# Kernel optimization log

Hardware: AMD Instinct MI355X
Metric: run time of the kernel (lower is better)

## Reference

```python
import jax, jax.numpy as jnp
from jax import lax
import numpy as np

B, H, W = 8, 512, 512
HW = H * W  # sentinel label for non-mask pixels


def _label_components(mask):
    """4-connectivity connected-component labeling (min flat-index per component).
    mask: [H,W] bool. Returns [HW] int32 labels; non-mask pixels get label HW.
    Label propagation + pointer jumping -> O(log diameter) iterations."""
    idx = jnp.arange(HW, dtype=jnp.int32).reshape(H, W)
    lab0 = jnp.where(mask, idx, HW)

    def step(lab):
        p = jnp.pad(lab, 1, mode='constant', constant_values=HW)
        nb = jnp.minimum(jnp.minimum(p[:-2, 1:-1], p[2:, 1:-1]),
                         jnp.minimum(p[1:-1, :-2], p[1:-1, 2:]))
        new = jnp.where(mask, jnp.minimum(lab, nb), HW)
        flat = new.reshape(-1)
        flat_ext = jnp.concatenate([flat, jnp.array([HW], dtype=flat.dtype)])
        new = jnp.minimum(flat, flat_ext[flat]).reshape(H, W)  # pointer jump
        return jnp.where(mask, new, HW)

    def cond(state):
        return state[1]

    def body(state):
        lab, _ = state
        new = step(lab)
        return new, jnp.any(new != lab)

    lab, _ = lax.while_loop(cond, body, (lab0, jnp.array(True)))
    return lab.reshape(-1)


def _keep_large(mask):
    """Keep pixels belonging to components with area > max_area/2 (matches
    ndi.label + ndi.sum + thresholded relabel; ndi.sum scaling by 255/1 cancels)."""
    labels = _label_components(mask)  # [HW]
    counts = jax.ops.segment_sum(mask.reshape(-1).astype(jnp.float32), labels,
                                 num_segments=HW + 1)  # counts[HW]=0 (non-mask contributes 0)
    max_area = counts.max()
    keep = mask.reshape(-1) & (counts[labels] > 0.5 * max_area)
    return keep.reshape(mask.shape)


def _masked_ce(logits, target):
    """CrossEntropyLoss(ignore_index=255, reduction='mean'). logits [B,C,H,W], target [B,H,W]."""
    logp = jax.nn.log_softmax(logits, axis=1)
    valid = target != 255
    tc = jnp.where(valid, target, 0)
    nll = -jnp.take_along_axis(logp, tc[:, None], axis=1)[:, 0]  # [B,H,W]
    denom = jnp.maximum(jnp.sum(valid), 1).astype(logp.dtype)
    return jnp.sum(jnp.where(valid, nll, 0.0)) / denom


def setup_inputs() -> dict:
    key = jax.random.key(0)
    k1, k2 = jax.random.split(key)
    preds = jax.random.normal(k1, (3, B, 2, H, W), dtype=jnp.float32)
    cams = jax.random.uniform(k2, (B, 1, H, W), dtype=jnp.float32)
    return {"preds": preds, "cams": cams}


def reference(preds, cams):
    cam = cams[:, 0]                      # [B,H,W]
    bg_mask = cam >= 0.2                  # pixels left at 255 in bg_label (the labeled regions)
    fg_mask = cam > 0.6                   # pixels set to 1 in fg_label
    keep_bg = jax.vmap(_keep_large)(bg_mask)
    keep_fg = jax.vmap(_keep_large)(fg_mask)
    bg_t = jnp.where(keep_bg, 255, 0).astype(jnp.int32)   # large uncertain regions ignored
    fg_t = jnp.where(keep_fg, 1, 255).astype(jnp.int32)   # small/non-fg ignored
    loss = jnp.float32(0.0)
    for i in range(preds.shape[0]):       # weight (1**i / 1) == 1
        loss = loss + _masked_ce(preds[i], fg_t) + _masked_ce(preds[i], bg_t)
    return loss
```

## Files before the change

### kernel.cpp

```cpp
#include <hip/hip_runtime.h>
#include <hip/hip_bf16.h>
#include <math.h>

#define Bsz    8
#define Wdim   512
#define HWv    (512 * 512)
#define LOG2HW 18
#define NIMG   16
#define TILE   64
#define TPIX   (TILE * TILE)


__device__ __forceinline__ int uf_find(int* L, int x) {
  int p = L[x];
  while (p != x) {
    int gp = L[p];
    if (gp != p) atomicMin(&L[x], gp);
    x = gp;
    p = L[x];
  }
  return x;
}

__device__ __forceinline__ int find_ro(const int* __restrict__ L, int x) {
  int p = L[x];
  while (p != x) { x = p; p = L[x]; }
  return x;
}

__device__ __forceinline__ void uf_union(int* L, int a, int b) {
  a = uf_find(L, a);
  b = uf_find(L, b);
  while (a != b) {
    if (a < b) { int t = a; a = b; b = t; }
    int old = atomicMin(&L[a], b);
    if (old == a) return;
    a = old;
  }
}


__global__ __launch_bounds__(1024) void k_local(const float* __restrict__ cams,
                                                int* __restrict__ labels,
                                                int* __restrict__ areas) {
  int img  = blockIdx.x >> 6;
  int tile = blockIdx.x & 63;
  int tY = tile >> 3, tX = tile & 7;
  int b = img & 7;
  bool fg = (img & 8) != 0;
  int gbase = img << LOG2HW;
  int oy = tY * TILE, ox = tX * TILE;
  int lane = threadIdx.x & 63;

  __shared__ int P[TPIX];
  __shared__ int A[TPIX];

  #pragma unroll
  for (int it = 0; it < 4; ++it) {
    int i  = it * 1024 + threadIdx.x;
    int ly = i >> 6;
    float c = cams[(b << LOG2HW) + ((oy + ly) << 9) + (ox + lane)];
    bool m = fg ? (c > 0.6f) : (c >= 0.2f);
    unsigned long long bm = __ballot(m);
    int par = -1;
    if (m) {
      unsigned long long below = (1ULL << lane) - 1ULL;
      unsigned long long z = (~bm) & below;
      int rs = z ? (64 - __clzll(z)) : 0;
      par = (ly << 6) + rs;
    }
    P[i] = par;
    A[i] = 0;
  }
  __syncthreads();

  #pragma unroll
  for (int it = 0; it < 4; ++it) {
    int i = it * 1024 + threadIdx.x;
    if (i >= TILE && P[i] >= 0 && P[i - TILE] >= 0) {
      bool skip = (lane > 0) && (P[i - 1] >= 0) && (P[i - TILE - 1] >= 0);
      if (!skip) uf_union(P, i, i - TILE);
    }
  }
  __syncthreads();

  #pragma unroll
  for (int it = 0; it < 4; ++it) {
    int i = it * 1024 + threadIdx.x;
    bool m = P[i] >= 0;
    unsigned long long bm = __ballot(m);
    int rs = 0;
    if (m) {
      unsigned long long below = (1ULL << lane) - 1ULL;
      unsigned long long z = (~bm) & below;
      rs = z ? (64 - __clzll(z)) : 0;
    }
    bool isStart = m && (rs == lane);
    int r = -1;
    if (isStart) r = find_ro(P, i);
    int root = __shfl(r, rs);
    if (m) P[i] = root;
    if (isStart) {
      unsigned long long t = (~bm) >> lane;
      int runlen = t ? (__ffsll((long long)t) - 1) : (64 - lane);
      atomicAdd(&A[root], runlen);
    }
  }
  __syncthreads();

  #pragma unroll
  for (int it = 0; it < 4; ++it) {
    int i  = it * 1024 + threadIdx.x;
    int ly = i >> 6;
    int g  = ((oy + ly) << 9) + (ox + lane);
    int p  = P[i];
    int lab = -1;
    if (p >= 0) lab = ((oy + (p >> 6)) << 9) + (ox + (p & 63));
    labels[gbase + g] = lab;
    areas[gbase + g]  = (p == i) ? A[i] : 0;
  }
}

__global__ void k_border(int* __restrict__ labels, int* __restrict__ maxa,
                         double* __restrict__ sums, int* __restrict__ counts) {
  if (blockIdx.x == 0) {
    if (threadIdx.x < NIMG) maxa[threadIdx.x] = 0;
    if (threadIdx.x < 2) { sums[threadIdx.x] = 0.0; counts[threadIdx.x] = 0; }
  }
  const int per_img = 14 * Wdim;
  int t = blockIdx.x * blockDim.x + threadIdx.x;
  if (t >= NIMG * per_img) return;
  int img = t / per_img;
  int r   = t - img * per_img;
  int k = r >> 9, j = r & (Wdim - 1);
  int* L = labels + (img << LOG2HW);
  if (k < 7) {
    int x = TILE * k + (TILE - 1);
    int p = (j << 9) + x, q = p + 1;
    if (L[p] >= 0 && L[q] >= 0) {
      bool skip = (j > 0) && (L[p - Wdim] >= 0) && (L[q - Wdim] >= 0);
      if (!skip) uf_union(L, p, q);
    }
  } else {
    int y = TILE * (k - 7) + (TILE - 1);
    int p = (y << 9) + j, q = p + Wdim;
    if (L[p] >= 0 && L[q] >= 0) {
      bool skip = (j > 0) && (L[p - 1] >= 0) && (L[q - 1] >= 0);
      if (!skip) uf_union(L, p, q);
    }
  }
}

__global__ void k_flatten(int* __restrict__ labels, int* __restrict__ areas) {
  int t = blockIdx.x * blockDim.x + threadIdx.x;
  int idx0 = t << 2;
  int4 ar = *(const int4*)&areas[idx0];
  if ((ar.x | ar.y | ar.z | ar.w) <= 0) return;
  int img  = idx0 >> LOG2HW;
  int base = img << LOG2HW;
  int* L = labels + base;
  int self0 = idx0 - base;
  int4 lab = *(const int4*)&labels[idx0];
  if (ar.x > 0) { int r = find_ro(L, lab.x); L[self0]     = r; if (r != self0)     atomicAdd(&areas[base + r], ar.x); }
  if (ar.y > 0) { int r = find_ro(L, lab.y); L[self0 + 1] = r; if (r != self0 + 1) atomicAdd(&areas[base + r], ar.y); }
  if (ar.z > 0) { int r = find_ro(L, lab.z); L[self0 + 2] = r; if (r != self0 + 2) atomicAdd(&areas[base + r], ar.z); }
  if (ar.w > 0) { int r = find_ro(L, lab.w); L[self0 + 3] = r; if (r != self0 + 3) atomicAdd(&areas[base + r], ar.w); }
}

__global__ void k_max(const int* __restrict__ areas, int* __restrict__ maxa) {
  int img = blockIdx.x >> 4;
  int seg = blockIdx.x & 15;
  const int4* a4 = (const int4*)(areas + (img << LOG2HW));
  int base = seg * (HWv / 4 / 16);
  int m = 0;
  #pragma unroll
  for (int k = 0; k < 16; ++k) {
    int4 v = a4[base + k * 256 + threadIdx.x];
    m = max(m, max(max(v.x, v.y), max(v.z, v.w)));
  }
  #pragma unroll
  for (int off = 32; off > 0; off >>= 1)
    m = max(m, __shfl_down(m, off));
  __shared__ int lm[4];
  int wave = threadIdx.x >> 6;
  if ((threadIdx.x & 63) == 0) lm[wave] = m;
  __syncthreads();
  if (threadIdx.x == 0) {
    int bm = max(max(lm[0], lm[1]), max(lm[2], lm[3]));
    if (bm > 0) atomicMax(&maxa[img], bm);
  }
}

__global__ __launch_bounds__(1024) void k_keepce(const float* __restrict__ preds,
                                                 const int* __restrict__ labels,
                                                 const int* __restrict__ areas,
                                                 const int* __restrict__ maxa,
                                                 double* __restrict__ sums,
                                                 int* __restrict__ counts) {
  int b    = blockIdx.x >> 6;
  int tile = blockIdx.x & 63;
  int tY = tile >> 3, tX = tile & 7;
  int oy = tY * TILE, ox = tX * TILE;
  int basebg = b << LOG2HW, basefg = (8 + b) << LOG2HW;
  int maxb = maxa[b], maxf = maxa[8 + b];

  __shared__ int Vbg[TPIX];
  __shared__ int Vfg[TPIX];

  int i  = threadIdx.x << 2;
  int ly = i >> 6, lx = i & 63;
  int g  = ((oy + ly) << 9) + (ox + lx);
  int4 lb = *(const int4*)&labels[basebg + g];
  int4 lf = *(const int4*)&labels[basefg + g];
  int4 ab = *(const int4*)&areas[basebg + g];
  int4 af = *(const int4*)&areas[basefg + g];
  if (ab.x > 0) { Vbg[i+0] = (2 * areas[basebg + lb.x] > maxb); lb.x = g + 0; }
  if (ab.y > 0) { Vbg[i+1] = (2 * areas[basebg + lb.y] > maxb); lb.y = g + 1; }
  if (ab.z > 0) { Vbg[i+2] = (2 * areas[basebg + lb.z] > maxb); lb.z = g + 2; }
  if (ab.w > 0) { Vbg[i+3] = (2 * areas[basebg + lb.w] > maxb); lb.w = g + 3; }
  if (af.x > 0) { Vfg[i+0] = (2 * areas[basefg + lf.x] > maxf); lf.x = g + 0; }
  if (af.y > 0) { Vfg[i+1] = (2 * areas[basefg + lf.y] > maxf); lf.y = g + 1; }
  if (af.z > 0) { Vfg[i+2] = (2 * areas[basefg + lf.z] > maxf); lf.z = g + 2; }
  if (af.w > 0) { Vfg[i+3] = (2 * areas[basefg + lf.w] > maxf); lf.w = g + 3; }
  __syncthreads();

  float4 A0[3], A1[3];
  #pragma unroll
  for (int p = 0; p < 3; p++) {
    const float* pb = preds + ((size_t)((p * Bsz + b) * 2) << LOG2HW);
    A0[p] = *(const float4*)&pb[g];
    A1[p] = *(const float4*)&pb[HWv + g];
  }
  int lbj[4] = {lb.x, lb.y, lb.z, lb.w};
  int lfj[4] = {lf.x, lf.y, lf.z, lf.w};
  bool vf[4], vb[4];
  #pragma unroll
  for (int j = 0; j < 4; j++) {
    int locb = (((lbj[j] >> 9) & 63) << 6) | (lbj[j] & 63);
    int locf = (((lfj[j] >> 9) & 63) << 6) | (lfj[j] & 63);
    bool kb = (lbj[j] >= 0) && (Vbg[locb] != 0);
    bool kf = (lfj[j] >= 0) && (Vfg[locf] != 0);
    vb[j] = !kb;
    vf[j] = kf;
  }
  int cf = (int)vf[0] + vf[1] + vf[2] + vf[3];
  int cb = (int)vb[0] + vb[1] + vb[2] + vb[3];
  float sfg = 0.f, sbg = 0.f;
  #pragma unroll
  for (int p = 0; p < 3; p++) {
    float d[4] = {A0[p].x - A1[p].x, A0[p].y - A1[p].y,
                  A0[p].z - A1[p].z, A0[p].w - A1[p].w};
    #pragma unroll
    for (int j = 0; j < 4; j++) {
      float sp = logf(1.f + expf(-fabsf(d[j])));
      sfg += vf[j] ? (fmaxf(d[j], 0.f) + sp) : 0.f;
      sbg += vb[j] ? (fmaxf(-d[j], 0.f) + sp) : 0.f;
    }
  }
  #pragma unroll
  for (int off = 32; off > 0; off >>= 1) {
    sfg += __shfl_down(sfg, off);
    sbg += __shfl_down(sbg, off);
    cf  += __shfl_down(cf, off);
    cb  += __shfl_down(cb, off);
  }
  __shared__ float lsf[16], lsb[16];
  __shared__ int   lcf[16], lcb[16];
  int wave = threadIdx.x >> 6;
  if ((threadIdx.x & 63) == 0) {
    lsf[wave] = sfg; lsb[wave] = sbg; lcf[wave] = cf; lcb[wave] = cb;
  }
  __syncthreads();
  if (threadIdx.x == 0) {
    float tf = 0.f, tb = 0.f; int af_ = 0, ab_ = 0;
    #pragma unroll
    for (int w = 0; w < 16; w++) { tf += lsf[w]; tb += lsb[w]; af_ += lcf[w]; ab_ += lcb[w]; }
    atomicAdd(&sums[0], (double)tf);
    atomicAdd(&sums[1], (double)tb);
    atomicAdd(&counts[0], af_);
    atomicAdd(&counts[1], ab_);
  }
}

__global__ void k_final(const double* __restrict__ sums, const int* __restrict__ counts,
                        float* __restrict__ out) {
  if (threadIdx.x == 0 && blockIdx.x == 0) {
    double df = counts[0] > 0 ? (double)counts[0] : 1.0;
    double db = counts[1] > 0 ? (double)counts[1] : 1.0;
    out[0] = (float)(sums[0] / df + sums[1] / db);
  }
}

extern "C" void kernel_launch(void* const* d_in, const int* in_sizes, int n_in,
                              void* d_out, int out_size, void* d_ws, size_t ws_size,
                              hipStream_t stream) {
  (void)in_sizes; (void)n_in; (void)out_size; (void)ws_size;
  const float* preds = (const float*)d_in[0];
  const float* cams  = (const float*)d_in[1];
  float* out = (float*)d_out;

  int* labels = (int*)d_ws;
  int* areas  = labels + NIMG * HWv;
  int* maxa   = areas + NIMG * HWv;
  double* sums = (double*)(maxa + 16);
  int* counts  = (int*)(sums + 2);

  const int threads = 256;

  k_local  <<<NIMG * 64, 1024, 0, stream>>>(cams, labels, areas);
  k_border <<<(NIMG * 14 * Wdim + threads - 1) / threads, threads, 0, stream>>>(labels, maxa, sums, counts);
  k_flatten<<<NIMG * HWv / (threads * 4), threads, 0, stream>>>(labels, areas);
  k_max    <<<NIMG * 16, threads, 0, stream>>>(areas, maxa);
  k_keepce <<<Bsz * 64, 1024, 0, stream>>>(preds, labels, areas, maxa, sums, counts);
  k_final  <<<1, 64, 0, stream>>>(sums, counts, out);
}
```

Baseline: 169.0 us.

## Split keep/CE kernel into per-image verdict bitmask pass and CE pass

```diff
diff --git a/kernel.cpp b/kernel.cpp
--- a/kernel.cpp
+++ b/kernel.cpp
@@ -191,72 +191,98 @@
   }
 }
 
-__global__ __launch_bounds__(1024) void k_keepce(const float* __restrict__ preds,
-                                                 const int* __restrict__ labels,
-                                                 const int* __restrict__ areas,
-                                                 const int* __restrict__ maxa,
-                                                 double* __restrict__ sums,
-                                                 int* __restrict__ counts) {
-  int b    = blockIdx.x >> 6;
+__global__ __launch_bounds__(1024) void k_verdict(const int* __restrict__ labels,
+                                                  const int* __restrict__ areas,
+                                                  const int* __restrict__ maxa,
+                                                  unsigned long long* __restrict__ bitsBG,
+                                                  unsigned long long* __restrict__ bitsFG) {
+  int img  = blockIdx.x >> 6;
   int tile = blockIdx.x & 63;
   int tY = tile >> 3, tX = tile & 7;
   int oy = tY * TILE, ox = tX * TILE;
-  int basebg = b << LOG2HW, basefg = (8 + b) << LOG2HW;
-  int maxb = maxa[b], maxf = maxa[8 + b];
-
-  __shared__ int Vbg[TPIX];
-  __shared__ int Vfg[TPIX];
+  int base = img << LOG2HW;
+  int mx = maxa[img];
+
+  __shared__ int V[TPIX];
 
   int i  = threadIdx.x << 2;
   int ly = i >> 6, lx = i & 63;
   int g  = ((oy + ly) << 9) + (ox + lx);
-  int4 lb = *(const int4*)&labels[basebg + g];
-  int4 lf = *(const int4*)&labels[basefg + g];
-  int4 ab = *(const int4*)&areas[basebg + g];
-  int4 af = *(const int4*)&areas[basefg + g];
-  if (ab.x > 0) { Vbg[i+0] = (2 * areas[basebg + lb.x] > maxb); lb.x = g + 0; }
-  if (ab.y > 0) { Vbg[i+1] = (2 * areas[basebg + lb.y] > maxb); lb.y = g + 1; }
-  if (ab.z > 0) { Vbg[i+2] = (2 * areas[basebg + lb.z] > maxb); lb.z = g + 2; }
-  if (ab.w > 0) { Vbg[i+3] = (2 * areas[basebg + lb.w] > maxb); lb.w = g + 3; }
-  if (af.x > 0) { Vfg[i+0] = (2 * areas[basefg + lf.x] > maxf); lf.x = g + 0; }
-  if (af.y > 0) { Vfg[i+1] = (2 * areas[basefg + lf.y] > maxf); lf.y = g + 1; }
-  if (af.z > 0) { Vfg[i+2] = (2 * areas[basefg + lf.z] > maxf); lf.z = g + 2; }
-  if (af.w > 0) { Vfg[i+3] = (2 * areas[basefg + lf.w] > maxf); lf.w = g + 3; }
-  __syncthreads();
-
-  float4 A0[3], A1[3];
-  #pragma unroll
-  for (int p = 0; p < 3; p++) {
-    const float* pb = preds + ((size_t)((p * Bsz + b) * 2) << LOG2HW);
-    A0[p] = *(const float4*)&pb[g];
-    A1[p] = *(const float4*)&pb[HWv + g];
-  }
-  int lbj[4] = {lb.x, lb.y, lb.z, lb.w};
-  int lfj[4] = {lf.x, lf.y, lf.z, lf.w};
-  bool vf[4], vb[4];
-  #pragma unroll
-  for (int j = 0; j < 4; j++) {
-    int locb = (((lbj[j] >> 9) & 63) << 6) | (lbj[j] & 63);
-    int locf = (((lfj[j] >> 9) & 63) << 6) | (lfj[j] & 63);
-    bool kb = (lbj[j] >= 0) && (Vbg[locb] != 0);
-    bool kf = (lfj[j] >= 0) && (Vfg[locf] != 0);
-    vb[j] = !kb;
-    vf[j] = kf;
-  }
-  int cf = (int)vf[0] + vf[1] + vf[2] + vf[3];
-  int cb = (int)vb[0] + vb[1] + vb[2] + vb[3];
+  int4 lb = *(const int4*)&labels[base + g];
+  int4 ar = *(const int4*)&areas[base + g];
+  if (ar.x > 0) { V[i + 0] = (2 * areas[base + lb.x] > mx); lb.x = g + 0; }
+  if (ar.y > 0) { V[i + 1] = (2 * areas[base + lb.y] > mx); lb.y = g + 1; }
+  if (ar.z > 0) { V[i + 2] = (2 * areas[base + lb.z] > mx); lb.z = g + 2; }
+  if (ar.w > 0) { V[i + 3] = (2 * areas[base + lb.w] > mx); lb.w = g + 3; }
+  __syncthreads();
+
+  int l[4] = {lb.x, lb.y, lb.z, lb.w};
+  unsigned nib = 0;
+  #pragma unroll
+  for (int j = 0; j < 4; ++j) {
+    if (l[j] >= 0) {
+      int loc = (((l[j] >> 9) & 63) << 6) | (l[j] & 63);
+      nib |= (V[loc] ? 1u : 0u) << j;
+    }
+  }
+
+  int lane = threadIdx.x & 63;
+  unsigned long long w = (unsigned long long)nib << ((lane & 15) << 2);
+  w |= __shfl_xor(w, 1);
+  w |= __shfl_xor(w, 2);
+  w |= __shfl_xor(w, 4);
+  w |= __shfl_xor(w, 8);
+  if ((lane & 15) == 0) {
+    int wordIdx = ((oy + ly) << 3) + tX;
+    unsigned long long* dst = (img < 8) ? (bitsBG + ((img & 7) << 12))
+                                        : (bitsFG + ((img & 7) << 12));
+    dst[wordIdx] = w;
+  }
+}
+
+__global__ __launch_bounds__(256) void k_ce(const float* __restrict__ preds,
+                                            const unsigned long long* __restrict__ bitsBG,
+                                            const unsigned long long* __restrict__ bitsFG,
+                                            double* __restrict__ sums,
+                                            int* __restrict__ counts) {
+  int tid = blockIdx.x * 256 + threadIdx.x;
+  int g4  = tid & 65535;
+  int b0  = tid >> 16;
+  int wi  = g4 >> 4;
+  int sh  = (g4 & 15) << 2;
+
+  unsigned long long wB0 = bitsBG[(b0 << 12) + wi];
+  unsigned long long wF0 = bitsFG[(b0 << 12) + wi];
+  unsigned long long wB1 = bitsBG[((b0 + 4) << 12) + wi];
+  unsigned long long wF1 = bitsFG[((b0 + 4) << 12) + wi];
+  unsigned nB[2] = { (unsigned)(wB0 >> sh) & 15u, (unsigned)(wB1 >> sh) & 15u };
+  unsigned nF[2] = { (unsigned)(wF0 >> sh) & 15u, (unsigned)(wF1 >> sh) & 15u };
+
+  int cf = __popc(nF[0]) + __popc(nF[1]);
+  int cb = 8 - __popc(nB[0]) - __popc(nB[1]);
+
   float sfg = 0.f, sbg = 0.f;
-  #pragma unroll
-  for (int p = 0; p < 3; p++) {
-    float d[4] = {A0[p].x - A1[p].x, A0[p].y - A1[p].y,
-                  A0[p].z - A1[p].z, A0[p].w - A1[p].w};
+  int px = g4 << 2;
+  #pragma unroll
+  for (int p = 0; p < 3; ++p) {
     #pragma unroll
-    for (int j = 0; j < 4; j++) {
-      float sp = logf(1.f + expf(-fabsf(d[j])));
-      sfg += vf[j] ? (fmaxf(d[j], 0.f) + sp) : 0.f;
-      sbg += vb[j] ? (fmaxf(-d[j], 0.f) + sp) : 0.f;
-    }
-  }
+    for (int bi = 0; bi < 2; ++bi) {
+      int b = b0 + 4 * bi;
+      const float* pb = preds + ((size_t)((p * Bsz + b) * 2) << LOG2HW);
+      float4 A0 = *(const float4*)&pb[px];
+      float4 A1 = *(const float4*)&pb[HWv + px];
+      float d[4] = {A0.x - A1.x, A0.y - A1.y, A0.z - A1.z, A0.w - A1.w};
+      #pragma unroll
+      for (int j = 0; j < 4; ++j) {
+        float sp = logf(1.f + expf(-fabsf(d[j])));
+        bool vfj = (nF[bi] >> j) & 1u;
+        bool vbj = !((nB[bi] >> j) & 1u);
+        sfg += vfj ? (fmaxf(d[j], 0.f) + sp) : 0.f;
+        sbg += vbj ? (fmaxf(-d[j], 0.f) + sp) : 0.f;
+      }
+    }
+  }
+
   #pragma unroll
   for (int off = 32; off > 0; off >>= 1) {
     sfg += __shfl_down(sfg, off);
@@ -264,17 +290,18 @@
     cf  += __shfl_down(cf, off);
     cb  += __shfl_down(cb, off);
   }
-  __shared__ float lsf[16], lsb[16];
-  __shared__ int   lcf[16], lcb[16];
+  __shared__ float lsf[4], lsb[4];
+  __shared__ int   lcf[4], lcb[4];
   int wave = threadIdx.x >> 6;
   if ((threadIdx.x & 63) == 0) {
     lsf[wave] = sfg; lsb[wave] = sbg; lcf[wave] = cf; lcb[wave] = cb;
   }
   __syncthreads();
   if (threadIdx.x == 0) {
-    float tf = 0.f, tb = 0.f; int af_ = 0, ab_ = 0;
-    #pragma unroll
-    for (int w = 0; w < 16; w++) { tf += lsf[w]; tb += lsb[w]; af_ += lcf[w]; ab_ += lcb[w]; }
+    float tf = lsf[0] + lsf[1] + lsf[2] + lsf[3];
+    float tb = lsb[0] + lsb[1] + lsb[2] + lsb[3];
+    int af_ = lcf[0] + lcf[1] + lcf[2] + lcf[3];
+    int ab_ = lcb[0] + lcb[1] + lcb[2] + lcb[3];
     atomicAdd(&sums[0], (double)tf);
     atomicAdd(&sums[1], (double)tb);
     atomicAdd(&counts[0], af_);
@@ -304,6 +331,8 @@
   int* maxa   = areas + NIMG * HWv;
   double* sums = (double*)(maxa + 16);
   int* counts  = (int*)(sums + 2);
+  unsigned long long* bitsBG = (unsigned long long*)(counts + 2);
+  unsigned long long* bitsFG = bitsBG + Bsz * (HWv / 64);
 
   const int threads = 256;
 
@@ -311,6 +340,7 @@
   k_border <<<(NIMG * 14 * Wdim + threads - 1) / threads, threads, 0, stream>>>(labels, maxa, sums, counts);
   k_flatten<<<NIMG * HWv / (threads * 4), threads, 0, stream>>>(labels, areas);
   k_max    <<<NIMG * 16, threads, 0, stream>>>(areas, maxa);
-  k_keepce <<<Bsz * 64, 1024, 0, stream>>>(preds, labels, areas, maxa, sums, counts);
+  k_verdict<<<NIMG * 64, 1024, 0, stream>>>(labels, areas, maxa, bitsBG, bitsFG);
+  k_ce     <<<1024, 256, 0, stream>>>(preds, bitsBG, bitsFG, sums, counts);
   k_final  <<<1, 64, 0, stream>>>(sums, counts, out);
 }
```

After: 199.8 us. +18.2%, slower.
